# Kernel tuning notes

Hardware: AMD Instinct MI355X
Metric: run time of the kernel (lower is better)

## Reference

```python
import jax, jax.numpy as jnp
import numpy as np
import math

NUM_CONVS = 4
GN_GROUPS = 32
GN_EPS = 1e-5
FPN_STRIDES = (8, 16, 32, 64, 128)
PRIOR_PROB = 0.01


def conv3x3(x, w, b):
    # x: [N,C,H,W], w: [O,I,3,3]
    y = jax.lax.conv_general_dilated(
        x, w, window_strides=(1, 1), padding='SAME',
        dimension_numbers=('NCHW', 'OIHW', 'NCHW'))
    return y + b[None, :, None, None]


def group_norm(x, gamma, beta):
    n, c, h, w = x.shape
    xg = x.reshape(n, GN_GROUPS, c // GN_GROUPS, h, w)
    mean = xg.mean(axis=(2, 3, 4), keepdims=True)
    var = xg.var(axis=(2, 3, 4), keepdims=True)
    xn = ((xg - mean) * jax.lax.rsqrt(var + GN_EPS)).reshape(n, c, h, w)
    return xn * gamma[None, :, None, None] + beta[None, :, None, None]


def subnet(x, ws, bs, gws, gbs):
    # NUM_CONVS x (conv3x3 -> GN -> ReLU)
    for i in range(NUM_CONVS):
        x = jax.nn.relu(group_norm(conv3x3(x, ws[i], bs[i]), gws[i], gbs[i]))
    return x


def permute_to_N_HWA_K(x, k):
    n = x.shape[0]
    return x.transpose(0, 2, 3, 1).reshape(n, -1, k)


def setup_inputs() -> dict:
    key = jax.random.key(0)
    ks = jax.random.split(key, 16)
    C, K = 256, 80
    feats = {
        'p3': jax.random.normal(ks[0], (1, C, 80, 80), jnp.float32),
        'p4': jax.random.normal(ks[1], (1, C, 40, 40), jnp.float32),
        'p5': jax.random.normal(ks[2], (1, C, 20, 20), jnp.float32),
        'p6': jax.random.normal(ks[3], (1, C, 10, 10), jnp.float32),
        'p7': jax.random.normal(ks[4], (1, C, 5, 5), jnp.float32),
    }
    std = 0.01
    bias_value = -math.log((1 - PRIOR_PROB) / PRIOR_PROB)
    params = {
        'cls_w': std * jax.random.normal(ks[5], (NUM_CONVS, C, C, 3, 3), jnp.float32),
        'cls_b': jnp.zeros((NUM_CONVS, C), jnp.float32),
        'cls_gn_w': jnp.ones((NUM_CONVS, C), jnp.float32),
        'cls_gn_b': jnp.zeros((NUM_CONVS, C), jnp.float32),
        'box_w': std * jax.random.normal(ks[6], (NUM_CONVS, C, C, 3, 3), jnp.float32),
        'box_b': jnp.zeros((NUM_CONVS, C), jnp.float32),
        'box_gn_w': jnp.ones((NUM_CONVS, C), jnp.float32),
        'box_gn_b': jnp.zeros((NUM_CONVS, C), jnp.float32),
        'score_w': std * jax.random.normal(ks[7], (K, C, 3, 3), jnp.float32),
        'score_b': jnp.full((K,), bias_value, jnp.float32),
        'pred_w': std * jax.random.normal(ks[8], (4, C, 3, 3), jnp.float32),
        'pred_b': jnp.zeros((4,), jnp.float32),
        'iou_w': std * jax.random.normal(ks[9], (1, C, 3, 3), jnp.float32),
        'iou_b': jnp.zeros((1,), jnp.float32),
        'scales': jnp.ones((5,), jnp.float32),
    }
    return {**feats, **params}


def reference(p3, p4, p5, p6, p7,
              cls_w, cls_b, cls_gn_w, cls_gn_b,
              box_w, box_b, box_gn_w, box_gn_b,
              score_w, score_b, pred_w, pred_b, iou_w, iou_b, scales):
    features = [p3, p4, p5, p6, p7]
    logits, bbox_reg, ious = [], [], []
    for l, feat in enumerate(features):
        c = subnet(feat, cls_w, cls_b, cls_gn_w, cls_gn_b)
        b = subnet(feat, box_w, box_b, box_gn_w, box_gn_b)
        logit = conv3x3(c, score_w, score_b)          # [N,80,H,W]
        iou = conv3x3(b, iou_w, iou_b)                # [N,1,H,W]
        bp = conv3x3(b, pred_w, pred_b) * scales[l]   # Scale module
        # norm_reg_targets=True branch
        reg = jax.nn.relu(bp) * FPN_STRIDES[l]        # [N,4,H,W]
        logits.append(permute_to_N_HWA_K(logit, 80))
        bbox_reg.append(permute_to_N_HWA_K(reg, 4))
        ious.append(permute_to_N_HWA_K(iou, 1))
    box_cls = jnp.concatenate(logits, axis=1)    # [N, sumHW, 80]
    box_delta = jnp.concatenate(bbox_reg, axis=1)  # [N, sumHW, 4]
    box_iou = jnp.concatenate(ious, axis=1)      # [N, sumHW, 1]
    # pack into one array for a single output: [N, sumHW, 85]
    return jnp.concatenate([box_cls, box_delta, box_iou], axis=-1)
```

## Files before the change

kernel.cpp:

```cpp
#include <hip/hip_runtime.h>

typedef unsigned short u16;
typedef __attribute__((ext_vector_type(8))) short bf16x8;
typedef __attribute__((ext_vector_type(4))) float f32x4;

#define NLEV 5
#define CCH 256
#define KTOT 2304
#define P_TOT 8525
#define PP_TOT 9165
#define PLS (PP_TOT*64)

__constant__ int   c_HW[NLEV]     = {6400, 1600, 400, 100, 25};
__constant__ int   c_W[NLEV]      = {80, 40, 20, 10, 5};
__constant__ int   c_off[NLEV]    = {0, 6400, 8000, 8400, 8500};
__constant__ int   c_poff[NLEV]   = {0, 6724, 8488, 8972, 9116};
__constant__ int   c_pts[NLEV+1]  = {0, 50, 63, 67, 68, 69};
__constant__ float c_stridef[NLEV]= {8.f, 16.f, 32.f, 64.f, 128.f};

__device__ __forceinline__ u16 f2bf(float f){
  union { float f; unsigned u; } v; v.f = f;
  unsigned r = v.u + 0x7fffu + ((v.u >> 16) & 1u);
  return (u16)(r >> 16);
}

__device__ __forceinline__ void g2l16(const u16* g, u16* l, int lane){
#if defined(__has_builtin)
#if __has_builtin(__builtin_amdgcn_global_load_lds)
  __builtin_amdgcn_global_load_lds(
      (const __attribute__((address_space(1))) unsigned int*)g,
      (__attribute__((address_space(3))) unsigned int*)l, 16, 0, 0);
  return;
#endif
#endif
  *(uint4*)(l + lane*8) = *(const uint4*)g;
}

#define WAIT_VM0_LGKM0 0x0070

template<int MODE>
__global__ __launch_bounds__(256, 2) void gemm_conv(
    const u16* __restrict__ Xc, const u16* __restrict__ Xb,
    const u16* __restrict__ Wc, const u16* __restrict__ Wb,
    const float* __restrict__ bc, const float* __restrict__ bb,
    float* __restrict__ Yc, float* __restrict__ Yb,
    float* __restrict__ stats,
    const float* __restrict__ predb, const float* __restrict__ ioub,
    const float* __restrict__ scales, float* __restrict__ out)
{
  __shared__ u16 sA0[8192], sB0[8192], sA1[8192], sB1[8192];
  __shared__ float sstat[16][2];

  const int ptile = blockIdx.x, mtile = blockIdx.y, br = blockIdx.z;
  int lv = 0;
  #pragma unroll
  for (int i = 1; i < NLEV; i++) if (ptile >= c_pts[i]) lv = i;
  const int ptl = ptile - c_pts[lv];
  const int HW = c_HW[lv], Wl = c_W[lv], wrow = Wl + 2;
  const int tid = threadIdx.x, wv = tid >> 6, ln = tid & 63;
  const int quad = ln >> 4, l15 = ln & 15;
  const int m0w = (wv & 1) * 64, n0w = (wv >> 1) * 64;

  const u16* __restrict__ X  = br ? Xb : Xc;
  const u16* __restrict__ WA = br ? Wb : Wc;

  const int ASTRIDE = (MODE == 0) ? 16384 : 8192;
  const u16* abase = WA + (size_t)(((MODE == 0) ? mtile*16 : 0) + wv*4)*512 + ln*8;

  const int bsw = ((ln & 7) ^ ((ln >> 3) & 7)) * 8;
  const u16* bsrc[4];
  #pragma unroll
  for (int i = 0; i < 4; i++) {
    const int p = ptl*128 + wv*32 + i*8 + (ln >> 3);
    int pb = 0;
    if (p < HW) { const int h = p / Wl, wi = p - h*Wl; pb = h*wrow + wi; }
    bsrc[i] = X + (size_t)(c_poff[lv] + pb) * 64 + bsw;
  }

  auto stage = [&](int s, u16* dA, u16* dB) {
    const int tap = s >> 2, cc = s & 3;
    const int dh = tap / 3, dw = tap - dh*3;
    const u16* as = abase + (size_t)s * ASTRIDE;
    const int bsh = cc * PLS + (dh*wrow + dw) * 64;
    u16* da = dA + (wv*4)*512;
    u16* db = dB + (wv*4)*512;
    #pragma unroll
    for (int i = 0; i < 4; i++) g2l16(as + i*512, da + i*512, ln);
    #pragma unroll
    for (int i = 0; i < 4; i++) g2l16(bsrc[i] + bsh, db + i*512, ln);
  };

  f32x4 acc[4][4];
  #pragma unroll
  for (int i = 0; i < 4; i++)
    #pragma unroll
    for (int j = 0; j < 4; j++) acc[i][j] = (f32x4){0.f, 0.f, 0.f, 0.f};

  if (MODE == 0 && tid < 32) sstat[tid >> 1][tid & 1] = 0.f;

  auto kbody = [&](int s, const u16* rA, const u16* rB, u16* wA2, u16* wB2) {
    __builtin_amdgcn_s_waitcnt(WAIT_VM0_LGKM0);
    __builtin_amdgcn_sched_barrier(0);
    __builtin_amdgcn_s_barrier();
    __builtin_amdgcn_sched_barrier(0);
    if (s < 35) stage(s + 1, wA2, wB2);
    bf16x8 af[2][4], bf[2][4];
    #pragma unroll
    for (int sub = 0; sub < 2; sub++) {
      #pragma unroll
      for (int t = 0; t < 4; t++) {
        const int swz = ((sub*4 + quad) ^ (l15 & 7)) * 8;
        af[sub][t] = *(const bf16x8*)&rA[(m0w + t*16 + l15)*64 + swz];
        bf[sub][t] = *(const bf16x8*)&rB[(n0w + t*16 + l15)*64 + swz];
      }
    }
    #pragma unroll
    for (int sub = 0; sub < 2; sub++)
      #pragma unroll
      for (int mt = 0; mt < 4; mt++)
        #pragma unroll
        for (int nt = 0; nt < 4; nt++)
          acc[mt][nt] = __builtin_amdgcn_mfma_f32_16x16x32_bf16(
              af[sub][mt], bf[sub][nt], acc[mt][nt], 0, 0, 0);
  };

  stage(0, sA0, sB0);
  #pragma unroll 1
  for (int s = 0; s < 36; s += 2) {
    kbody(s,     sA0, sB0, sA1, sB1);
    kbody(s + 1, sA1, sB1, sA0, sB0);
  }

  const int nrem = HW - ptl*128;
  if (MODE == 0) {
    const float* __restrict__ bias = br ? bb : bc;
    float* __restrict__ Y = br ? Yb : Yc;
    #pragma unroll
    for (int mt = 0; mt < 4; mt++) {
      const int mloc = m0w + mt*16 + quad*4;
      const int mrow = mtile*128 + mloc;
      const f32x4 bv = *(const f32x4*)&bias[mrow];
      float s = 0.f, sq = 0.f;
      #pragma unroll
      for (int nt = 0; nt < 4; nt++) {
        const int nl = n0w + nt*16 + l15;
        f32x4 v = acc[mt][nt] + bv;
        if (nl < nrem) {
          const size_t n = (size_t)(c_off[lv] + ptl*128 + nl);
          *(f32x4*)&Y[n*CCH + mrow] = v;
          #pragma unroll
          for (int r = 0; r < 4; r++) { s += v[r]; sq += v[r]*v[r]; }
        }
      }
      #pragma unroll
      for (int o = 1; o < 16; o <<= 1) { s += __shfl_xor(s, o); sq += __shfl_xor(sq, o); }
      if (l15 == 0) {
        const int g = mloc >> 3;
        atomicAdd(&sstat[g][0], s);
        atomicAdd(&sstat[g][1], sq);
      }
    }
    __syncthreads();
    if (tid < 32) {
      const int g = tid >> 1, c = tid & 1;
      atomicAdd(&stats[((br*NLEV + lv)*32 + mtile*16 + g)*2 + c], sstat[g][c]);
    }
  } else {
    const float scl = scales[lv];
    const float stf = c_stridef[lv];
    #pragma unroll
    for (int mt = 0; mt < 4; mt++) {
      const int mr0 = m0w + mt*16 + quad*4;
      if (mr0 >= 85) continue;
      #pragma unroll
      for (int nt = 0; nt < 4; nt++) {
        const int nl = n0w + nt*16 + l15;
        if (nl >= nrem) continue;
        const size_t n = (size_t)(c_off[lv] + ptl*128 + nl);
        const f32x4 v = acc[mt][nt];
        #pragma unroll
        for (int r = 0; r < 4; r++) {
          const int m = mr0 + r;
          if (br == 0) {
            if (m < 80) out[n*85 + m] = v[r] + bc[m];
          } else {
            if (m < 4) {
              const float t = (v[r] + predb[m]) * scl;
              out[n*85 + 80 + m] = fmaxf(t, 0.f) * stf;
            } else if (m == 4) {
              out[n*85 + 84] = v[r] + ioub[0];
            }
          }
        }
      }
    }
  }
}

__global__ __launch_bounds__(256) void gn_relu(
    const float* __restrict__ Yc, const float* __restrict__ Yb,
    const float* __restrict__ stats,
    const float* __restrict__ gwc, const float* __restrict__ gbc,
    const float* __restrict__ gwb, const float* __restrict__ gbb,
    u16* __restrict__ Xc, u16* __restrict__ Xb)
{
  const int t = blockIdx.x * 256 + threadIdx.x;
  if (t >= 2 * P_TOT * 32) return;
  const int br = t / (P_TOT * 32);
  const int r  = t - br * (P_TOT * 32);
  const int pg = r >> 5;
  const int c0 = (r & 31) << 3;
  int lv = 0;
  #pragma unroll
  for (int i = 1; i < NLEV; i++) if (pg >= c_off[i]) lv = i;
  const int pl = pg - c_off[lv];
  const int Wl = c_W[lv];
  const int g = c0 >> 3;
  const float* st = &stats[(((size_t)br*NLEV + lv)*32 + g)*2];
  const float cnt = 8.f * (float)c_HW[lv];
  const float mean = st[0] / cnt;
  const float var  = st[1] / cnt - mean*mean;
  const float rstd = rsqrtf(var + 1e-5f);
  const float* Y  = br ? Yb : Yc;
  const float* gw = br ? gwb : gwc;
  const float* gb = br ? gbb : gbc;
  u16* X = br ? Xb : Xc;
  const float* y = &Y[(size_t)pg*CCH + c0];
  const int h = pl / Wl, wi = pl - h*Wl;
  const size_t pidx = (size_t)(c_poff[lv] + (h+1)*(Wl+2) + (wi+1));
  union { u16 u[8]; uint4 v; } pk;
  #pragma unroll
  for (int i = 0; i < 8; i++) {
    const float v = (y[i] - mean)*rstd*gw[c0+i] + gb[c0+i];
    pk.u[i] = f2bf(fmaxf(v, 0.f));
  }
  *(uint4*)&X[(size_t)(c0 >> 6)*PLS + pidx*64 + (c0 & 63)] = pk.v;
}

__global__ __launch_bounds__(256) void feat2bf(
    const float* __restrict__ p3, const float* __restrict__ p4,
    const float* __restrict__ p5, const float* __restrict__ p6,
    const float* __restrict__ p7, u16* __restrict__ X)
{
  const int t = blockIdx.x * 256 + threadIdx.x;
  if (t >= P_TOT * 32) return;
  const int pg = t >> 5, c0 = (t & 31) << 3;
  int lv = 0;
  #pragma unroll
  for (int i = 1; i < NLEV; i++) if (pg >= c_off[i]) lv = i;
  const int pl = pg - c_off[lv];
  const float* src = lv==0 ? p3 : lv==1 ? p4 : lv==2 ? p5 : lv==3 ? p6 : p7;
  const int HW = c_HW[lv], Wl = c_W[lv];
  const int h = pl / Wl, wi = pl - h*Wl;
  const size_t pidx = (size_t)(c_poff[lv] + (h+1)*(Wl+2) + (wi+1));
  union { u16 u[8]; uint4 v; } pk;
  #pragma unroll
  for (int i = 0; i < 8; i++)
    pk.u[i] = f2bf(src[(size_t)(c0+i)*HW + pl]);
  *(uint4*)&X[(size_t)(c0 >> 6)*PLS + pidx*64 + (c0 & 63)] = pk.v;
}

__global__ __launch_bounds__(256) void wconv(
    const float* __restrict__ cw, const float* __restrict__ bw,
    u16* __restrict__ Wc, u16* __restrict__ Wb)
{
  const size_t N = (size_t)4*256*KTOT;
  const size_t t = (size_t)blockIdx.x * 256 + threadIdx.x;
  if (t >= 2*N) return;
  const float* src = (t < N) ? cw : bw;
  u16* dst = (t < N) ? Wc : Wb;
  const size_t i = (t < N) ? t : t - N;
  const size_t lc = i / KTOT;
  const int kk = (int)(i - lc*KTOT);
  const int l = (int)(lc >> 8), co = (int)(lc & 255);
  const int tap = kk >> 8, ci = kk & 255;
  const int s = kk >> 6, kl = kk & 63;
  const int r = co & 7, p = (kl >> 3) ^ r;
  const size_t d = (size_t)l*589824 +
      ((size_t)((s*32 + (co >> 3))*64 + r*8 + p))*8 + (kl & 7);
  dst[d] = f2bf(src[(lc*256 + ci)*9 + tap]);
}

__global__ __launch_bounds__(256) void hconv(
    const float* __restrict__ sw, const float* __restrict__ pw,
    const float* __restrict__ iw, u16* __restrict__ Whc, u16* __restrict__ Whb)
{
  const int N = 128 * KTOT;
  const int t = blockIdx.x * 256 + threadIdx.x;
  if (t >= 2*N) return;
  const int i = (t < N) ? t : t - N;
  const int co = i / KTOT, kk = i - co*KTOT;
  const int tap = kk >> 8, ci = kk & 255;
  const int s = kk >> 6, kl = kk & 63;
  const int r = co & 7, p = (kl >> 3) ^ r;
  const size_t d = ((size_t)((s*16 + (co >> 3))*64 + r*8 + p))*8 + (kl & 7);
  float v = 0.f;
  if (t < N) {
    if (co < 80) v = sw[(co*256 + ci)*9 + tap];
    Whc[d] = f2bf(v);
  } else {
    if (co < 4)       v = pw[(co*256 + ci)*9 + tap];
    else if (co == 4) v = iw[ci*9 + tap];
    Whb[d] = f2bf(v);
  }
}

extern "C" void kernel_launch(void* const* d_in, const int* in_sizes, int n_in,
                              void* d_out, int out_size, void* d_ws, size_t ws_size,
                              hipStream_t stream)
{
  const float* p3      = (const float*)d_in[0];
  const float* p4      = (const float*)d_in[1];
  const float* p5      = (const float*)d_in[2];
  const float* p6      = (const float*)d_in[3];
  const float* p7      = (const float*)d_in[4];
  const float* cls_w   = (const float*)d_in[5];
  const float* cls_b   = (const float*)d_in[6];
  const float* cls_gw  = (const float*)d_in[7];
  const float* cls_gb  = (const float*)d_in[8];
  const float* box_w   = (const float*)d_in[9];
  const float* box_b   = (const float*)d_in[10];
  const float* box_gw  = (const float*)d_in[11];
  const float* box_gb  = (const float*)d_in[12];
  const float* score_w = (const float*)d_in[13];
  const float* score_b = (const float*)d_in[14];
  const float* pred_w  = (const float*)d_in[15];
  const float* pred_b  = (const float*)d_in[16];
  const float* iou_w   = (const float*)d_in[17];
  const float* iou_b   = (const float*)d_in[18];
  const float* scales  = (const float*)d_in[19];
  float* out = (float*)d_out;

  char* w = (char*)d_ws;
  size_t o = 0;
  auto alloc = [&](size_t b) { void* p = w + o; o += (b + 255) & ~(size_t)255; return p; };
  u16*   XF = (u16*)alloc((size_t)PP_TOT*CCH*2);
  u16*   XC = (u16*)alloc((size_t)PP_TOT*CCH*2);
  u16*   XB = (u16*)alloc((size_t)PP_TOT*CCH*2);
  float* ST = (float*)alloc((size_t)4*2*NLEV*32*2*4);
  u16*  WRC = (u16*)alloc((size_t)4*256*KTOT*2);
  u16*  WRB = (u16*)alloc((size_t)4*256*KTOT*2);
  u16*  WHC = (u16*)alloc((size_t)128*KTOT*2);
  u16*  WHB = (u16*)alloc((size_t)128*KTOT*2);
  float* YC = (float*)alloc((size_t)P_TOT*CCH*4);
  float* YB = (float*)alloc((size_t)P_TOT*CCH*4);

  hipMemsetAsync(XF, 0, (size_t)3*PP_TOT*CCH*2 + (size_t)4*2*NLEV*32*2*4, stream);

  wconv<<<dim3((unsigned)(((size_t)2*4*256*KTOT + 255)/256)), 256, 0, stream>>>(cls_w, box_w, WRC, WRB);
  hconv<<<dim3((2*128*KTOT + 255)/256), 256, 0, stream>>>(score_w, pred_w, iou_w, WHC, WHB);
  feat2bf<<<dim3((P_TOT*32 + 255)/256), 256, 0, stream>>>(p3, p4, p5, p6, p7, XF);

  const u16* xci = XF; const u16* xbi = XF;
  for (int l = 0; l < 4; l++) {
    float* STl = ST + (size_t)l*2*NLEV*32*2;
    gemm_conv<0><<<dim3(69, 2, 2), 256, 0, stream>>>(
        xci, xbi, WRC + (size_t)l*589824, WRB + (size_t)l*589824,
        cls_b + l*256, box_b + l*256, YC, YB, STl,
        nullptr, nullptr, nullptr, nullptr);
    gn_relu<<<dim3((2*P_TOT*32 + 255)/256), 256, 0, stream>>>(
        YC, YB, STl, cls_gw + l*256, cls_gb + l*256, box_gw + l*256, box_gb + l*256,
        XC, XB);
    xci = XC; xbi = XB;
  }
  gemm_conv<1><<<dim3(69, 1, 2), 256, 0, stream>>>(
      xci, xbi, WHC, WHB, score_b, nullptr, nullptr, nullptr, nullptr,
      pred_b, iou_b, scales, out);
}
```

Baseline: 367.6 us.

## Split conv GEMMs along K into two halves with separate stats and head reduction

Result: slower. 386.8 us (+5.2%).

```diff
diff --git a/kernel.cpp b/kernel.cpp
--- a/kernel.cpp
+++ b/kernel.cpp
@@ -16,6 +16,7 @@
 __constant__ int   c_off[NLEV]    = {0, 6400, 8000, 8400, 8500};
 __constant__ int   c_poff[NLEV]   = {0, 6724, 8488, 8972, 9116};
 __constant__ int   c_pts[NLEV+1]  = {0, 50, 63, 67, 68, 69};
+__constant__ int   c_pts64[NLEV+1]= {0, 100, 125, 132, 134, 135};
 __constant__ float c_stridef[NLEV]= {8.f, 16.f, 32.f, 64.f, 128.f};
 
 __device__ __forceinline__ u16 f2bf(float f){
@@ -42,24 +43,28 @@
 __global__ __launch_bounds__(256, 2) void gemm_conv(
     const u16* __restrict__ Xc, const u16* __restrict__ Xb,
     const u16* __restrict__ Wc, const u16* __restrict__ Wb,
-    const float* __restrict__ bc, const float* __restrict__ bb,
-    float* __restrict__ Yc, float* __restrict__ Yb,
-    float* __restrict__ stats,
-    const float* __restrict__ predb, const float* __restrict__ ioub,
-    const float* __restrict__ scales, float* __restrict__ out)
-{
+    float* __restrict__ Y0c, float* __restrict__ Y1c,
+    float* __restrict__ Y0b, float* __restrict__ Y1b,
+    float* __restrict__ OP)
+{
+  constexpr int NT  = (MODE == 0) ? 4 : 2;
+  constexpr int NBS = (MODE == 0) ? 4 : 2;
+  constexpr int BNp = (MODE == 0) ? 128 : 64;
   __shared__ u16 sA0[8192], sB0[8192], sA1[8192], sB1[8192];
-  __shared__ float sstat[16][2];
-
-  const int ptile = blockIdx.x, mtile = blockIdx.y, br = blockIdx.z;
+
+  const int ptile = blockIdx.x;
+  const int mtile = (MODE == 0) ? blockIdx.y : 0;
+  const int kh = blockIdx.z >> 1, br = blockIdx.z & 1;
+  const int* pts = (MODE == 0) ? c_pts : c_pts64;
   int lv = 0;
   #pragma unroll
-  for (int i = 1; i < NLEV; i++) if (ptile >= c_pts[i]) lv = i;
-  const int ptl = ptile - c_pts[lv];
+  for (int i = 1; i < NLEV; i++) if (ptile >= pts[i]) lv = i;
+  const int ptl = ptile - pts[lv];
   const int HW = c_HW[lv], Wl = c_W[lv], wrow = Wl + 2;
   const int tid = threadIdx.x, wv = tid >> 6, ln = tid & 63;
-  const int quad = ln >> 4, l15 = ln & 15;
-  const int m0w = (wv & 1) * 64, n0w = (wv >> 1) * 64;
+  const int quad = ln >> 4, l15 = ln & 15, lr = ln >> 3;
+  const int m0w = (wv & 1) * 64;
+  const int n0w = (wv >> 1) * ((MODE == 0) ? 64 : 32);
 
   const u16* __restrict__ X  = br ? Xb : Xc;
   const u16* __restrict__ WA = br ? Wb : Wc;
@@ -67,139 +72,151 @@
   const int ASTRIDE = (MODE == 0) ? 16384 : 8192;
   const u16* abase = WA + (size_t)(((MODE == 0) ? mtile*16 : 0) + wv*4)*512 + ln*8;
 
-  const int bsw = ((ln & 7) ^ ((ln >> 3) & 7)) * 8;
-  const u16* bsrc[4];
-  #pragma unroll
-  for (int i = 0; i < 4; i++) {
-    const int p = ptl*128 + wv*32 + i*8 + (ln >> 3);
+  const int bsw = ((ln & 7) ^ (lr & 7)) * 8;
+  const u16* bsrc[NBS];
+  #pragma unroll
+  for (int j = 0; j < NBS; j++) {
+    const int p = ptl*BNp + wv*(8*NBS) + j*8 + lr;
     int pb = 0;
     if (p < HW) { const int h = p / Wl, wi = p - h*Wl; pb = h*wrow + wi; }
-    bsrc[i] = X + (size_t)(c_poff[lv] + pb) * 64 + bsw;
-  }
-
-  auto stage = [&](int s, u16* dA, u16* dB) {
+    bsrc[j] = X + (size_t)(c_poff[lv] + pb) * 64 + bsw;
+  }
+
+  auto stage = [&](int t, u16* dA, u16* dB) {
+    const int s = kh*18 + t;
     const int tap = s >> 2, cc = s & 3;
     const int dh = tap / 3, dw = tap - dh*3;
     const u16* as = abase + (size_t)s * ASTRIDE;
     const int bsh = cc * PLS + (dh*wrow + dw) * 64;
     u16* da = dA + (wv*4)*512;
-    u16* db = dB + (wv*4)*512;
-    #pragma unroll
-    for (int i = 0; i < 4; i++) g2l16(as + i*512, da + i*512, ln);
-    #pragma unroll
-    for (int i = 0; i < 4; i++) g2l16(bsrc[i] + bsh, db + i*512, ln);
+    u16* db = dB + (wv*NBS)*512;
+    #pragma unroll
+    for (int j = 0; j < 4; j++) g2l16(as + j*512, da + j*512, ln);
+    #pragma unroll
+    for (int j = 0; j < NBS; j++) g2l16(bsrc[j] + bsh, db + j*512, ln);
   };
 
-  f32x4 acc[4][4];
+  f32x4 acc[4][NT];
   #pragma unroll
   for (int i = 0; i < 4; i++)
     #pragma unroll
-    for (int j = 0; j < 4; j++) acc[i][j] = (f32x4){0.f, 0.f, 0.f, 0.f};
-
-  if (MODE == 0 && tid < 32) sstat[tid >> 1][tid & 1] = 0.f;
-
-  auto kbody = [&](int s, const u16* rA, const u16* rB, u16* wA2, u16* wB2) {
+    for (int j = 0; j < NT; j++) acc[i][j] = (f32x4){0.f, 0.f, 0.f, 0.f};
+
+  auto kbody = [&](int t, const u16* rA, const u16* rB, u16* wA2, u16* wB2) {
+    __builtin_amdgcn_sched_barrier(0);
     __builtin_amdgcn_s_waitcnt(WAIT_VM0_LGKM0);
     __builtin_amdgcn_sched_barrier(0);
     __builtin_amdgcn_s_barrier();
     __builtin_amdgcn_sched_barrier(0);
-    if (s < 35) stage(s + 1, wA2, wB2);
-    bf16x8 af[2][4], bf[2][4];
+    if (t < 17) stage(t + 1, wA2, wB2);
+    bf16x8 af[2][4], bf[2][NT];
     #pragma unroll
     for (int sub = 0; sub < 2; sub++) {
-      #pragma unroll
-      for (int t = 0; t < 4; t++) {
-        const int swz = ((sub*4 + quad) ^ (l15 & 7)) * 8;
-        af[sub][t] = *(const bf16x8*)&rA[(m0w + t*16 + l15)*64 + swz];
-        bf[sub][t] = *(const bf16x8*)&rB[(n0w + t*16 + l15)*64 + swz];
-      }
+      const int swz = ((sub*4 + quad) ^ (l15 & 7)) * 8;
+      #pragma unroll
+      for (int mt = 0; mt < 4; mt++)
+        af[sub][mt] = *(const bf16x8*)&rA[(m0w + mt*16 + l15)*64 + swz];
+      #pragma unroll
+      for (int nt = 0; nt < NT; nt++)
+        bf[sub][nt] = *(const bf16x8*)&rB[(n0w + nt*16 + l15)*64 + swz];
     }
     #pragma unroll
     for (int sub = 0; sub < 2; sub++)
       #pragma unroll
       for (int mt = 0; mt < 4; mt++)
         #pragma unroll
-        for (int nt = 0; nt < 4; nt++)
+        for (int nt = 0; nt < NT; nt++)
           acc[mt][nt] = __builtin_amdgcn_mfma_f32_16x16x32_bf16(
               af[sub][mt], bf[sub][nt], acc[mt][nt], 0, 0, 0);
   };
 
   stage(0, sA0, sB0);
   #pragma unroll 1
-  for (int s = 0; s < 36; s += 2) {
-    kbody(s,     sA0, sB0, sA1, sB1);
-    kbody(s + 1, sA1, sB1, sA0, sB0);
-  }
-
-  const int nrem = HW - ptl*128;
+  for (int t = 0; t < 18; t += 2) {
+    kbody(t,     sA0, sB0, sA1, sB1);
+    kbody(t + 1, sA1, sB1, sA0, sB0);
+  }
+
+  const int nrem = HW - ptl*BNp;
   if (MODE == 0) {
-    const float* __restrict__ bias = br ? bb : bc;
-    float* __restrict__ Y = br ? Yb : Yc;
+    float* __restrict__ Y = kh ? (br ? Y1b : Y1c) : (br ? Y0b : Y0c);
     #pragma unroll
     for (int mt = 0; mt < 4; mt++) {
-      const int mloc = m0w + mt*16 + quad*4;
-      const int mrow = mtile*128 + mloc;
-      const f32x4 bv = *(const f32x4*)&bias[mrow];
-      float s = 0.f, sq = 0.f;
-      #pragma unroll
-      for (int nt = 0; nt < 4; nt++) {
+      const int mrow = mtile*128 + m0w + mt*16 + quad*4;
+      #pragma unroll
+      for (int nt = 0; nt < NT; nt++) {
         const int nl = n0w + nt*16 + l15;
-        f32x4 v = acc[mt][nt] + bv;
         if (nl < nrem) {
-          const size_t n = (size_t)(c_off[lv] + ptl*128 + nl);
-          *(f32x4*)&Y[n*CCH + mrow] = v;
-          #pragma unroll
-          for (int r = 0; r < 4; r++) { s += v[r]; sq += v[r]*v[r]; }
-        }
-      }
-      #pragma unroll
-      for (int o = 1; o < 16; o <<= 1) { s += __shfl_xor(s, o); sq += __shfl_xor(sq, o); }
-      if (l15 == 0) {
-        const int g = mloc >> 3;
-        atomicAdd(&sstat[g][0], s);
-        atomicAdd(&sstat[g][1], sq);
-      }
-    }
-    __syncthreads();
-    if (tid < 32) {
-      const int g = tid >> 1, c = tid & 1;
-      atomicAdd(&stats[((br*NLEV + lv)*32 + mtile*16 + g)*2 + c], sstat[g][c]);
-    }
-  } else {
-    const float scl = scales[lv];
-    const float stf = c_stridef[lv];
-    #pragma unroll
-    for (int mt = 0; mt < 4; mt++) {
-      const int mr0 = m0w + mt*16 + quad*4;
-      if (mr0 >= 85) continue;
-      #pragma unroll
-      for (int nt = 0; nt < 4; nt++) {
-        const int nl = n0w + nt*16 + l15;
-        if (nl >= nrem) continue;
-        const size_t n = (size_t)(c_off[lv] + ptl*128 + nl);
-        const f32x4 v = acc[mt][nt];
-        #pragma unroll
-        for (int r = 0; r < 4; r++) {
-          const int m = mr0 + r;
-          if (br == 0) {
-            if (m < 80) out[n*85 + m] = v[r] + bc[m];
-          } else {
-            if (m < 4) {
-              const float t = (v[r] + predb[m]) * scl;
-              out[n*85 + 80 + m] = fmaxf(t, 0.f) * stf;
-            } else if (m == 4) {
-              out[n*85 + 84] = v[r] + ioub[0];
-            }
-          }
+          const size_t n = (size_t)(c_off[lv] + ptl*BNp + nl);
+          *(f32x4*)&Y[n*CCH + mrow] = acc[mt][nt];
         }
       }
     }
-  }
+  } else {
+    float* __restrict__ O = OP + (size_t)(br*2 + kh) * P_TOT * 128;
+    #pragma unroll
+    for (int mt = 0; mt < 4; mt++) {
+      const int mr0 = m0w + mt*16 + quad*4;
+      #pragma unroll
+      for (int nt = 0; nt < NT; nt++) {
+        const int nl = n0w + nt*16 + l15;
+        if (nl < nrem) {
+          const size_t n = (size_t)(c_off[lv] + ptl*BNp + nl);
+          *(f32x4*)&O[n*128 + mr0] = acc[mt][nt];
+        }
+      }
+    }
+  }
+}
+
+__global__ __launch_bounds__(256) void gn_stats2(
+    const float* __restrict__ Y0c, const float* __restrict__ Y1c,
+    const float* __restrict__ Y0b, const float* __restrict__ Y1b,
+    const float* __restrict__ bc, const float* __restrict__ bb,
+    float* __restrict__ stats)
+{
+  __shared__ float sstat[32][2];
+  const int blk = blockIdx.x, br = blockIdx.y;
+  int lv = 0;
+  #pragma unroll
+  for (int i = 1; i < NLEV; i++) if (blk >= c_pts64[i]) lv = i;
+  const int pl0 = (blk - c_pts64[lv]) * 64;
+  const int HW = c_HW[lv];
+  const int t = threadIdx.x, g = t & 31, pr = t >> 5;
+  const float* __restrict__ Y0 = br ? Y0b : Y0c;
+  const float* __restrict__ Y1 = br ? Y1b : Y1c;
+  const float* __restrict__ bias = br ? bb : bc;
+  const f32x4 b0 = *(const f32x4*)&bias[g*8];
+  const f32x4 b1 = *(const f32x4*)&bias[g*8 + 4];
+  float s = 0.f, sq = 0.f;
+  #pragma unroll
+  for (int i = 0; i < 8; i++) {
+    const int pl = pl0 + pr + i*8;
+    if (pl < HW) {
+      const size_t base = (size_t)(c_off[lv] + pl) * CCH + g*8;
+      const f32x4 a0 = *(const f32x4*)&Y0[base]     + *(const f32x4*)&Y1[base]     + b0;
+      const f32x4 a1 = *(const f32x4*)&Y0[base + 4] + *(const f32x4*)&Y1[base + 4] + b1;
+      #pragma unroll
+      for (int r = 0; r < 4; r++) {
+        s  += a0[r] + a1[r];
+        sq += a0[r]*a0[r] + a1[r]*a1[r];
+      }
+    }
+  }
+  if (t < 64) sstat[t >> 1][t & 1] = 0.f;
+  __syncthreads();
+  atomicAdd(&sstat[g][0], s);
+  atomicAdd(&sstat[g][1], sq);
+  __syncthreads();
+  if (t < 64)
+    atomicAdd(&stats[((br*NLEV + lv)*32 + (t >> 1))*2 + (t & 1)], sstat[t >> 1][t & 1]);
 }
 
 __global__ __launch_bounds__(256) void gn_relu(
-    const float* __restrict__ Yc, const float* __restrict__ Yb,
+    const float* __restrict__ Y0c, const float* __restrict__ Y1c,
+    const float* __restrict__ Y0b, const float* __restrict__ Y1b,
     const float* __restrict__ stats,
+    const float* __restrict__ bc, const float* __restrict__ bb,
     const float* __restrict__ gwc, const float* __restrict__ gbc,
     const float* __restrict__ gwb, const float* __restrict__ gbb,
     u16* __restrict__ Xc, u16* __restrict__ Xb)
@@ -221,20 +238,49 @@
   const float mean = st[0] / cnt;
   const float var  = st[1] / cnt - mean*mean;
   const float rstd = rsqrtf(var + 1e-5f);
-  const float* Y  = br ? Yb : Yc;
+  const float* Y0 = br ? Y0b : Y0c;
+  const float* Y1 = br ? Y1b : Y1c;
+  const float* bs = br ? bb : bc;
   const float* gw = br ? gwb : gwc;
   const float* gb = br ? gbb : gbc;
   u16* X = br ? Xb : Xc;
-  const float* y = &Y[(size_t)pg*CCH + c0];
+  const float* y0 = &Y0[(size_t)pg*CCH + c0];
+  const float* y1 = &Y1[(size_t)pg*CCH + c0];
   const int h = pl / Wl, wi = pl - h*Wl;
   const size_t pidx = (size_t)(c_poff[lv] + (h+1)*(Wl+2) + (wi+1));
   union { u16 u[8]; uint4 v; } pk;
   #pragma unroll
   for (int i = 0; i < 8; i++) {
-    const float v = (y[i] - mean)*rstd*gw[c0+i] + gb[c0+i];
+    const float v = (y0[i] + y1[i] + bs[c0+i] - mean)*rstd*gw[c0+i] + gb[c0+i];
     pk.u[i] = f2bf(fmaxf(v, 0.f));
   }
   *(uint4*)&X[(size_t)(c0 >> 6)*PLS + pidx*64 + (c0 & 63)] = pk.v;
+}
+
+__global__ __launch_bounds__(256) void head_out(
+    const float* __restrict__ OP,
+    const float* __restrict__ score_b, const float* __restrict__ pred_b,
+    const float* __restrict__ iou_b, const float* __restrict__ scales,
+    float* __restrict__ out)
+{
+  const int t = blockIdx.x * 256 + threadIdx.x;
+  if (t >= P_TOT * 96) return;
+  const int n = t / 96, m = t - n*96;
+  if (m >= 85) return;
+  int lv = 0;
+  #pragma unroll
+  for (int i = 1; i < NLEV; i++) if (n >= c_off[i]) lv = i;
+  const size_t S = (size_t)P_TOT * 128;
+  const size_t r = (size_t)n * 128;
+  if (m < 80) {
+    out[(size_t)n*85 + m] = OP[r + m] + OP[S + r + m] + score_b[m];
+  } else if (m < 84) {
+    const int mm = m - 80;
+    float v = (OP[2*S + r + mm] + OP[3*S + r + mm] + pred_b[mm]) * scales[lv];
+    out[(size_t)n*85 + 80 + mm] = fmaxf(v, 0.f) * c_stridef[lv];
+  } else {
+    out[(size_t)n*85 + 84] = OP[2*S + r + 4] + OP[3*S + r + 4] + iou_b[0];
+  }
 }
 
 __global__ __launch_bounds__(256) void feat2bf(
@@ -342,8 +388,11 @@
   u16*  WRB = (u16*)alloc((size_t)4*256*KTOT*2);
   u16*  WHC = (u16*)alloc((size_t)128*KTOT*2);
   u16*  WHB = (u16*)alloc((size_t)128*KTOT*2);
-  float* YC = (float*)alloc((size_t)P_TOT*CCH*4);
-  float* YB = (float*)alloc((size_t)P_TOT*CCH*4);
+  float* Y0C = (float*)alloc((size_t)P_TOT*CCH*4);
+  float* Y1C = (float*)alloc((size_t)P_TOT*CCH*4);
+  float* Y0B = (float*)alloc((size_t)P_TOT*CCH*4);
+  float* Y1B = (float*)alloc((size_t)P_TOT*CCH*4);
+  float* OP  = (float*)alloc((size_t)4*P_TOT*128*4);
 
   hipMemsetAsync(XF, 0, (size_t)3*PP_TOT*CCH*2 + (size_t)4*2*NLEV*32*2*4, stream);
 
@@ -354,16 +403,19 @@
   const u16* xci = XF; const u16* xbi = XF;
   for (int l = 0; l < 4; l++) {
     float* STl = ST + (size_t)l*2*NLEV*32*2;
-    gemm_conv<0><<<dim3(69, 2, 2), 256, 0, stream>>>(
+    gemm_conv<0><<<dim3(69, 2, 4), 256, 0, stream>>>(
         xci, xbi, WRC + (size_t)l*589824, WRB + (size_t)l*589824,
-        cls_b + l*256, box_b + l*256, YC, YB, STl,
-        nullptr, nullptr, nullptr, nullptr);
+        Y0C, Y1C, Y0B, Y1B, nullptr);
+    gn_stats2<<<dim3(135, 2), 256, 0, stream>>>(
+        Y0C, Y1C, Y0B, Y1B, cls_b + l*256, box_b + l*256, STl);
     gn_relu<<<dim3((2*P_TOT*32 + 255)/256), 256, 0, stream>>>(
-        YC, YB, STl, cls_gw + l*256, cls_gb + l*256, box_gw + l*256, box_gb + l*256,
+        Y0C, Y1C, Y0B, Y1B, STl, cls_b + l*256, box_b + l*256,
+        cls_gw + l*256, cls_gb + l*256, box_gw + l*256, box_gb + l*256,
         XC, XB);
     xci = XC; xbi = XB;
   }
-  gemm_conv<1><<<dim3(69, 1, 2), 256, 0, stream>>>(
-      xci, xbi, WHC, WHB, score_b, nullptr, nullptr, nullptr, nullptr,
-      pred_b, iou_b, scales, out);
-}
+  gemm_conv<1><<<dim3(135, 1, 4), 256, 0, stream>>>(
+      xci, xbi, WHC, WHB, nullptr, nullptr, nullptr, nullptr, OP);
+  head_out<<<dim3((P_TOT*96 + 255)/256), 256, 0, stream>>>(
+      OP, score_b, pred_b, iou_b, scales, out);
+}
```

## Tile output as 2D 8x16 pixel blocks with shared halo tile reused across taps

Applied to the files above, without the earlier changes.

Result: no change. 367.0 us (-0.2%).

```diff
diff --git a/kernel.cpp b/kernel.cpp
--- a/kernel.cpp
+++ b/kernel.cpp
@@ -15,7 +15,8 @@
 __constant__ int   c_W[NLEV]      = {80, 40, 20, 10, 5};
 __constant__ int   c_off[NLEV]    = {0, 6400, 8000, 8400, 8500};
 __constant__ int   c_poff[NLEV]   = {0, 6724, 8488, 8972, 9116};
-__constant__ int   c_pts[NLEV+1]  = {0, 50, 63, 67, 68, 69};
+__constant__ int   c_tls[NLEV+1]  = {0, 50, 65, 71, 73, 74};
+__constant__ int   c_ntx[NLEV]    = {5, 3, 2, 1, 1};
 __constant__ float c_stridef[NLEV]= {8.f, 16.f, 32.f, 64.f, 128.f};
 
 __device__ __forceinline__ u16 f2bf(float f){
@@ -48,18 +49,25 @@
     const float* __restrict__ predb, const float* __restrict__ ioub,
     const float* __restrict__ scales, float* __restrict__ out)
 {
-  __shared__ u16 sA0[8192], sB0[8192], sA1[8192], sB1[8192];
+  __shared__ u16 sA0[8192], sA1[8192];
+  __shared__ u16 hB0[23*512], hB1[23*512];
   __shared__ float sstat[16][2];
 
-  const int ptile = blockIdx.x, mtile = blockIdx.y, br = blockIdx.z;
+  const int ptile = blockIdx.x;
+  const int mtile = (MODE == 0) ? blockIdx.y : 0;
+  const int br = blockIdx.z;
   int lv = 0;
   #pragma unroll
-  for (int i = 1; i < NLEV; i++) if (ptile >= c_pts[i]) lv = i;
-  const int ptl = ptile - c_pts[lv];
-  const int HW = c_HW[lv], Wl = c_W[lv], wrow = Wl + 2;
+  for (int i = 1; i < NLEV; i++) if (ptile >= c_tls[i]) lv = i;
+  const int tidx = ptile - c_tls[lv];
+  const int ntx = c_ntx[lv];
+  const int ty0 = (tidx / ntx) * 8, tx0 = (tidx - (tidx / ntx) * ntx) * 16;
+  const int W = c_W[lv], wrow2 = W + 2;
+
   const int tid = threadIdx.x, wv = tid >> 6, ln = tid & 63;
   const int quad = ln >> 4, l15 = ln & 15;
-  const int m0w = (wv & 1) * 64, n0w = (wv >> 1) * 64;
+  const int m0w = (wv & 1) * 64;
+  const int pyw = (wv >> 1) * 4;
 
   const u16* __restrict__ X  = br ? Xb : Xc;
   const u16* __restrict__ WA = br ? Wb : Wc;
@@ -67,28 +75,32 @@
   const int ASTRIDE = (MODE == 0) ? 16384 : 8192;
   const u16* abase = WA + (size_t)(((MODE == 0) ? mtile*16 : 0) + wv*4)*512 + ln*8;
 
-  const int bsw = ((ln & 7) ^ ((ln >> 3) & 7)) * 8;
-  const u16* bsrc[4];
-  #pragma unroll
-  for (int i = 0; i < 4; i++) {
-    const int p = ptl*128 + wv*32 + i*8 + (ln >> 3);
-    int pb = 0;
-    if (p < HW) { const int h = p / Wl, wi = p - h*Wl; pb = h*wrow + wi; }
-    bsrc[i] = X + (size_t)(c_poff[lv] + pb) * 64 + bsw;
-  }
-
-  auto stage = [&](int s, u16* dA, u16* dB) {
-    const int tap = s >> 2, cc = s & 3;
-    const int dh = tap / 3, dw = tap - dh*3;
-    const u16* as = abase + (size_t)s * ASTRIDE;
-    const int bsh = cc * PLS + (dh*wrow + dw) * 64;
+  const u16* hptr[6]; int hnum = 0;
+  #pragma unroll
+  for (int i = 0; i < 6; i++) {
+    const int j = wv + 4*i;
+    if (j < 23) {
+      const int item = j*64 + ln;
+      int hp = item >> 3; if (hp >= 180) hp -= 180;
+      const int g = item & 7;
+      const int hy = hp / 18, hx = hp - hy*18;
+      const int prow = c_poff[lv] + (ty0 + hy)*wrow2 + tx0 + hx;
+      hptr[i] = X + (size_t)prow*64 + ((g ^ (hp & 7)) << 3);
+      hnum = i + 1;
+    }
+  }
+
+  auto stageA = [&](int cc, int tap, u16* dA) {
+    const u16* as = abase + (size_t)(tap*4 + cc) * ASTRIDE;
     u16* da = dA + (wv*4)*512;
-    u16* db = dB + (wv*4)*512;
-    #pragma unroll
-    for (int i = 0; i < 4; i++) g2l16(as + i*512, da + i*512, ln);
-    #pragma unroll
-    for (int i = 0; i < 4; i++) g2l16(bsrc[i] + bsh, db + i*512, ln);
+    #pragma unroll
+    for (int j = 0; j < 4; j++) g2l16(as + j*512, da + j*512, ln);
   };
+  auto stageH = [&](int cc, u16* dH) {
+    const size_t cof = (size_t)cc * PLS;
+    for (int i = 0; i < hnum; i++)
+      g2l16(hptr[i] + cof, dH + (wv + 4*i)*512, ln);
+  };
 
   f32x4 acc[4][4];
   #pragma unroll
@@ -98,20 +110,32 @@
 
   if (MODE == 0 && tid < 32) sstat[tid >> 1][tid & 1] = 0.f;
 
-  auto kbody = [&](int s, const u16* rA, const u16* rB, u16* wA2, u16* wB2) {
+  auto kbody = [&](int t, const u16* rA, u16* wA2) {
+    __builtin_amdgcn_sched_barrier(0);
     __builtin_amdgcn_s_waitcnt(WAIT_VM0_LGKM0);
     __builtin_amdgcn_sched_barrier(0);
     __builtin_amdgcn_s_barrier();
     __builtin_amdgcn_sched_barrier(0);
-    if (s < 35) stage(s + 1, wA2, wB2);
+    const int cc = t / 9, tap = t - cc*9;
+    if (t < 35) {
+      const int t1 = t + 1, ncc = t1 / 9;
+      stageA(ncc, t1 - ncc*9, wA2);
+    }
+    if (tap == 8 && cc < 3) stageH(cc + 1, ((cc + 1) & 1) ? hB1 : hB0);
+    const u16* rB = (cc & 1) ? hB1 : hB0;
+    const int dh = tap / 3, dw = tap - dh*3;
     bf16x8 af[2][4], bf[2][4];
     #pragma unroll
     for (int sub = 0; sub < 2; sub++) {
-      #pragma unroll
-      for (int t = 0; t < 4; t++) {
-        const int swz = ((sub*4 + quad) ^ (l15 & 7)) * 8;
-        af[sub][t] = *(const bf16x8*)&rA[(m0w + t*16 + l15)*64 + swz];
-        bf[sub][t] = *(const bf16x8*)&rB[(n0w + t*16 + l15)*64 + swz];
+      const int swzA = ((sub*4 + quad) ^ (l15 & 7)) * 8;
+      #pragma unroll
+      for (int mt = 0; mt < 4; mt++)
+        af[sub][mt] = *(const bf16x8*)&rA[(m0w + mt*16 + l15)*64 + swzA];
+      #pragma unroll
+      for (int nt = 0; nt < 4; nt++) {
+        const int hp = (pyw + nt + dh)*18 + l15 + dw;
+        const int gk = sub*4 + quad;
+        bf[sub][nt] = *(const bf16x8*)&rB[hp*64 + ((gk ^ (hp & 7)) << 3)];
       }
     }
     #pragma unroll
@@ -124,14 +148,15 @@
               af[sub][mt], bf[sub][nt], acc[mt][nt], 0, 0, 0);
   };
 
-  stage(0, sA0, sB0);
+  stageH(0, hB0);
+  stageA(0, 0, sA0);
   #pragma unroll 1
-  for (int s = 0; s < 36; s += 2) {
-    kbody(s,     sA0, sB0, sA1, sB1);
-    kbody(s + 1, sA1, sB1, sA0, sB0);
-  }
-
-  const int nrem = HW - ptl*128;
+  for (int t = 0; t < 36; t += 2) {
+    kbody(t,     sA0, sA1);
+    kbody(t + 1, sA1, sA0);
+  }
+
+  const int gx = tx0 + l15;
   if (MODE == 0) {
     const float* __restrict__ bias = br ? bb : bc;
     float* __restrict__ Y = br ? Yb : Yc;
@@ -143,10 +168,10 @@
       float s = 0.f, sq = 0.f;
       #pragma unroll
       for (int nt = 0; nt < 4; nt++) {
-        const int nl = n0w + nt*16 + l15;
+        const int gy = ty0 + pyw + nt;
         f32x4 v = acc[mt][nt] + bv;
-        if (nl < nrem) {
-          const size_t n = (size_t)(c_off[lv] + ptl*128 + nl);
+        if (gy < W && gx < W) {
+          const size_t n = (size_t)(c_off[lv] + gy*W + gx);
           *(f32x4*)&Y[n*CCH + mrow] = v;
           #pragma unroll
           for (int r = 0; r < 4; r++) { s += v[r]; sq += v[r]*v[r]; }
@@ -174,9 +199,9 @@
       if (mr0 >= 85) continue;
       #pragma unroll
       for (int nt = 0; nt < 4; nt++) {
-        const int nl = n0w + nt*16 + l15;
-        if (nl >= nrem) continue;
-        const size_t n = (size_t)(c_off[lv] + ptl*128 + nl);
+        const int gy = ty0 + pyw + nt;
+        if (gy >= W || gx >= W) continue;
+        const size_t n = (size_t)(c_off[lv] + gy*W + gx);
         const f32x4 v = acc[mt][nt];
         #pragma unroll
         for (int r = 0; r < 4; r++) {
@@ -354,7 +379,7 @@
   const u16* xci = XF; const u16* xbi = XF;
   for (int l = 0; l < 4; l++) {
     float* STl = ST + (size_t)l*2*NLEV*32*2;
-    gemm_conv<0><<<dim3(69, 2, 2), 256, 0, stream>>>(
+    gemm_conv<0><<<dim3(74, 2, 2), 256, 0, stream>>>(
         xci, xbi, WRC + (size_t)l*589824, WRB + (size_t)l*589824,
         cls_b + l*256, box_b + l*256, YC, YB, STl,
         nullptr, nullptr, nullptr, nullptr);
@@ -363,7 +388,7 @@
         XC, XB);
     xci = XC; xbi = XB;
   }
-  gemm_conv<1><<<dim3(69, 1, 2), 256, 0, stream>>>(
+  gemm_conv<1><<<dim3(74, 1, 2), 256, 0, stream>>>(
       xci, xbi, WHC, WHB, score_b, nullptr, nullptr, nullptr, nullptr,
       pred_b, iou_b, scales, out);
 }
```
